# Kernel tuning notes

Hardware: AMD Instinct MI355X
Metric: run time of the kernel (lower is better)

## Reference

```python
import jax, jax.numpy as jnp
import numpy as np

D = 1024      # d_model
H = 16        # nhead
DH = 64       # qkv_dim (per-head)
FF = 4096     # dim_feedforward
EPS = 1e-5


def layer_norm(x, g, b):
    mu = jnp.mean(x, axis=-1, keepdims=True)
    var = jnp.mean(jnp.square(x - mu), axis=-1, keepdims=True)
    return (x - mu) * jax.lax.rsqrt(var + EPS) * g + b


def setup_inputs() -> dict:
    key = jax.random.key(0)
    ks = jax.random.split(key, 17)
    s = 0.02
    inp = {
        "src": jax.random.normal(ks[0], (2, 2048, D), jnp.float32),
        "qw": jax.random.normal(ks[1], (H * DH, D), jnp.float32) * s,
        "qb": jnp.zeros((H * DH,), jnp.float32),
        "kw": jax.random.normal(ks[2], (H * DH, D), jnp.float32) * s,
        "kb": jnp.zeros((H * DH,), jnp.float32),
        "vw": jax.random.normal(ks[3], (H * DH, D), jnp.float32) * s,
        "vb": jnp.zeros((H * DH,), jnp.float32),
        "ow": jax.random.normal(ks[4], (D, H * DH), jnp.float32) * s,
        "ob": jnp.zeros((D,), jnp.float32),
        "w1": jax.random.normal(ks[5], (FF, D), jnp.float32) * s,
        "b1": jnp.zeros((FF,), jnp.float32),
        "w2": jax.random.normal(ks[6], (D, FF), jnp.float32) * s,
        "b2": jnp.zeros((D,), jnp.float32),
        "g1": jnp.ones((D,), jnp.float32),
        "beta1": jnp.zeros((D,), jnp.float32),
        "g2": jnp.ones((D,), jnp.float32),
        "beta2": jnp.zeros((D,), jnp.float32),
    }
    return inp


def _attn(x, qw, qb, kw, kb, vw, vb, ow, ob):
    B, S, _ = x.shape
    scale = 1.0 / np.sqrt(DH)
    # projections -> [B, H, S, DH]
    q = (x @ qw.T + qb).reshape(B, S, H, DH).transpose(0, 2, 1, 3)
    k = (x @ kw.T + kb).reshape(B, S, H, DH).transpose(0, 2, 1, 3)
    v = (x @ vw.T + vb).reshape(B, S, H, DH).transpose(0, 2, 1, 3)
    scores = jnp.einsum('bhsd,bhtd->bhst', q, k) * scale
    attn = jax.nn.softmax(scores, axis=-1)
    out = jnp.einsum('bhst,bhtd->bhsd', attn, v)  # [B,H,S,DH]
    out = out.transpose(0, 2, 1, 3).reshape(B, S, H * DH)
    return out @ ow.T + ob


def reference(src, qw, qb, kw, kb, vw, vb, ow, ob, w1, b1, w2, b2, g1, beta1, g2, beta2):
    x = src
    # post-LN (norm_first=False), dropout=0 (eval)
    x = layer_norm(x + _attn(x, qw, qb, kw, kb, vw, vb, ow, ob), g1, beta1)
    ff = jax.nn.relu(x @ w1.T + b1) @ w2.T + b2
    x = layer_norm(x + ff, g2, beta2)
    return x
```

## Files before the change

### kernel.cpp

```cpp
#include <hip/hip_runtime.h>

typedef unsigned short bf16_t;
typedef unsigned short u16x8 __attribute__((ext_vector_type(8)));
typedef unsigned short u16x4 __attribute__((ext_vector_type(4)));
typedef float f32x4 __attribute__((ext_vector_type(4)));

#define D_MODEL 1024
#define NHEAD 16
#define DHEAD 64
#define FF_DIM 4096
#define SEQ 2048
#define BATCH 2
#define LOG2E 1.44269504088896340736f
#define EXP2F(x) __builtin_amdgcn_exp2f(x)

#define GLOAD_LDS16(gp, lp)                                          \
  __builtin_amdgcn_global_load_lds(                                  \
      (const __attribute__((address_space(1))) void*)(gp),           \
      (__attribute__((address_space(3))) void*)(lp), 16, 0, 0)

static __device__ __forceinline__ float bf2f(bf16_t b) {
  union { unsigned u; float f; } x;
  x.u = ((unsigned)b) << 16;
  return x.f;
}
static __device__ __forceinline__ bf16_t f2bf(float f) {
  union { float f; unsigned u; } x;
  x.f = f;
  unsigned r = (x.u + 0x7fffu + ((x.u >> 16) & 1u)) >> 16;
  return (bf16_t)r;
}
static __device__ __forceinline__ int cvtpk(float lo, float hi) {
  int r;
  asm("v_cvt_pk_bf16_f32 %0, %1, %2" : "=v"(r) : "v"(lo), "v"(hi));
  return r;
}
static __device__ __forceinline__ f32x4 mfma16(u16x8 a, u16x8 b, f32x4 c) {
  return __builtin_amdgcn_mfma_f32_16x16x32_bf16(a, b, c, 0, 0, 0);
}
static __device__ __forceinline__ u16x8 load8_f32(const float* q) {
  const float4 v0 = *(const float4*)(q);
  const float4 v1 = *(const float4*)(q + 4);
  u16x8 r;
  r[0] = f2bf(v0.x); r[1] = f2bf(v0.y); r[2] = f2bf(v0.z); r[3] = f2bf(v0.w);
  r[4] = f2bf(v1.x); r[5] = f2bf(v1.y); r[6] = f2bf(v1.z); r[7] = f2bf(v1.w);
  return r;
}

__global__ __launch_bounds__(256) void cvt_f32_bf16(
    const float* __restrict__ in, bf16_t* __restrict__ out, long n) {
  const long i = ((long)blockIdx.x * 256 + threadIdx.x) * 8;
  if (i < n) *(u16x8*)(out + i) = load8_f32(in + i);
}

template <int SMODE>
__global__ __launch_bounds__(256) void gemm_lds(
    const bf16_t* __restrict__ A, const bf16_t* __restrict__ W,
    const float* __restrict__ bq_, const float* __restrict__ bk_,
    const float* __restrict__ bv_, bf16_t* __restrict__ C0,
    bf16_t* __restrict__ C1, bf16_t* __restrict__ C2,
    bf16_t* __restrict__ C3,
    int N, int Kseg, long lda, long ldw, int relu, float qscale,
    int gxs) {
  __shared__ bf16_t As[128 * 32];
  __shared__ bf16_t Bs[128 * 32];
  const int tid = threadIdx.x;
  const int lane = tid & 63;
  const int w = tid >> 6;
  const int wr = w >> 1, wc = w & 1;
  const int g = lane >> 4, c = lane & 15;

  const int per = (int)gridDim.x >> 3;
  const int gt = (blockIdx.x & 7) * per + (blockIdx.x >> 3);
  const int u = gt & 31;
  const int st = gt >> 5;
  const int sx = st % gxs;
  const int t2 = st / gxs;
  const int sy = t2 & 7;
  const int z = t2 >> 3;
  const long bm = (long)(sy * 4 + (u & 3)) * 128;
  const long bn = (long)(sx * 8 + (u >> 2)) * 128;
  const long koff = (long)z * Kseg;

  f32x4 acc[4][4];
#pragma unroll
  for (int i = 0; i < 4; ++i)
#pragma unroll
    for (int j = 0; j < 4; ++j) acc[i][j] = (f32x4){0.f, 0.f, 0.f, 0.f};

  for (int k0 = 0; k0 < Kseg; k0 += 32) {
    __syncthreads();
#pragma unroll
    for (int ld = 0; ld < 2; ++ld) {
      const int ch = ld * 256 + tid;
      GLOAD_LDS16(A + (bm + (ch >> 2)) * lda + koff + k0 + (ch & 3) * 8,
                  As + (ld * 256 + w * 64) * 8);
    }
#pragma unroll
    for (int ld = 0; ld < 2; ++ld) {
      const int ch = ld * 256 + tid;
      GLOAD_LDS16(W + (bn + (ch >> 2)) * ldw + koff + k0 + (ch & 3) * 8,
                  Bs + (ld * 256 + w * 64) * 8);
    }
    __syncthreads();
    u16x8 af[4], bfv[4];
#pragma unroll
    for (int i = 0; i < 4; ++i)
      af[i] = *(const u16x8*)(As + (wr * 64 + i * 16 + c) * 32 + g * 8);
#pragma unroll
    for (int j = 0; j < 4; ++j)
      bfv[j] = *(const u16x8*)(Bs + (wc * 64 + j * 16 + c) * 32 + g * 8);
    __builtin_amdgcn_s_setprio(1);
#pragma unroll
    for (int i = 0; i < 4; ++i)
#pragma unroll
      for (int j = 0; j < 4; ++j) acc[i][j] = mfma16(af[i], bfv[j], acc[i][j]);
    __builtin_amdgcn_s_setprio(0);
  }

  bf16_t* __restrict__ pp =
      (z == 0) ? C0 : (z == 1) ? C1 : (z == 2) ? C2 : C3;
#pragma unroll
  for (int i = 0; i < 4; ++i) {
#pragma unroll
    for (int j = 0; j < 4; ++j) {
      const int nn = (int)bn + wc * 64 + j * 16 + c;
#pragma unroll
      for (int r = 0; r < 4; ++r) {
        const int mm = (int)bm + wr * 64 + i * 16 + g * 4 + r;
        if (SMODE == 0) {
          float v = acc[i][j][r] + bq_[nn];
          if (relu) v = fmaxf(v, 0.f);
          C0[(long)mm * N + nn] = f2bf(v);
        } else if (SMODE == 4) {
          pp[(long)mm * N + nn] = f2bf(acc[i][j][r]);
        } else {
          const int seg = nn >> 10;
          const int col = nn & 1023;
          const int h = col >> 6, dh = col & 63;
          const int b = mm >> 11, s = mm & 2047;
          if (seg == 0) {
            const float v = (acc[i][j][r] + bq_[col]) * qscale;
            C0[((((long)b * NHEAD + h) * SEQ + s) << 6) + dh] = f2bf(v);
          } else if (seg == 1) {
            const float v = acc[i][j][r] + bk_[col];
            C1[((((long)b * NHEAD + h) * SEQ + s) << 6) + dh] = f2bf(v);
          } else {
            const float v = acc[i][j][r] + bv_[col];
            C2[(((long)b * NHEAD + h) * DHEAD + dh) * SEQ + s] = f2bf(v);
          }
        }
      }
    }
  }
}

template <int KEY>
static __device__ __forceinline__ void stage_tile(
    const bf16_t* __restrict__ gbase, long rstride, bf16_t* lds,
    int tid, int w) {
#pragma unroll
  for (int i = 0; i < 2; ++i) {
    const int row = i * 32 + (tid >> 3);
    const int key = KEY ? ((row & 3) | ((row & 8) >> 1)) : (row & 7);
    const int c4 = (tid & 7) ^ key;
    GLOAD_LDS16(gbase + (long)row * rstride + c4 * 8,
                lds + (i * 256 + w * 64) * 8);
  }
}

__global__ __launch_bounds__(256, 2) void attn_fwd(
    const bf16_t* __restrict__ Q, const bf16_t* __restrict__ K,
    const bf16_t* __restrict__ Vt, bf16_t* __restrict__ O) {
  __shared__ bf16_t Ks0[64 * 64];
  __shared__ bf16_t Ks1[64 * 64];
  __shared__ bf16_t Vs0[64 * 64];
  __shared__ bf16_t Vs1[64 * 64];
  const int tid = threadIdx.x;
  const int lane = tid & 63;
  const int w = tid >> 6;
  const int g = lane >> 4, c = lane & 15;
  const int lb = blockIdx.x;
  const int xcd = lb & 7, sl = lb >> 3;
  const int bh = xcd * 4 + (sl >> 4);
  const int q0 = (sl & 15) * 128 + w * 32;
  const bf16_t* Qb = Q + (long)bh * SEQ * DHEAD;
  const bf16_t* Kb = K + (long)bh * SEQ * DHEAD;
  const bf16_t* Vb = Vt + (long)bh * DHEAD * SEQ;

  u16x8 bq[2][2];
#pragma unroll
  for (int qh = 0; qh < 2; ++qh) {
    bq[qh][0] = *(const u16x8*)(Qb + (q0 + qh * 16 + c) * DHEAD + g * 8);
    bq[qh][1] = *(const u16x8*)(Qb + (q0 + qh * 16 + c) * DHEAD + 32 + g * 8);
  }

  float m0 = -1e30f, m1 = -1e30f, lp0 = 0.f, lp1 = 0.f;
  f32x4 oacc[4][2];
#pragma unroll
  for (int d = 0; d < 4; ++d)
#pragma unroll
    for (int qh = 0; qh < 2; ++qh) oacc[d][qh] = (f32x4){0.f, 0.f, 0.f, 0.f};

  const int ck = c & 7;
  const int pr = ((c >> 2) << 3) | (c & 3);

  for (int t0 = 0; t0 < SEQ; t0 += 128) {
    __syncthreads();
    stage_tile<1>(Kb + (long)t0 * DHEAD, DHEAD, Ks0, tid, w);
    stage_tile<1>(Kb + (long)(t0 + 64) * DHEAD, DHEAD, Ks1, tid, w);
    stage_tile<0>(Vb + t0, SEQ, Vs0, tid, w);
    stage_tile<0>(Vb + t0 + 64, SEQ, Vs1, tid, w);
    __syncthreads();

#pragma unroll
    for (int sub = 0; sub < 2; ++sub) {
      const bf16_t* Ks = sub ? Ks1 : Ks0;
      const bf16_t* Vs = sub ? Vs1 : Vs0;

      f32x4 s[2][2][2];
#pragma unroll
      for (int tt = 0; tt < 2; ++tt) {
        const int rowA = (tt * 32 + pr) * 64;
        const int rowC = (tt * 32 + pr + 4) * 64;
        const u16x8 kA = *(const u16x8*)(Ks + rowA + (g ^ ck) * 8);
        const u16x8 kB = *(const u16x8*)(Ks + rowA + ((4 + g) ^ ck) * 8);
        const u16x8 kC = *(const u16x8*)(Ks + rowC + (g ^ ck) * 8);
        const u16x8 kD = *(const u16x8*)(Ks + rowC + ((4 + g) ^ ck) * 8);
        __builtin_amdgcn_s_setprio(1);
#pragma unroll
        for (int qh = 0; qh < 2; ++qh) {
          s[tt][0][qh] = mfma16(kA, bq[qh][0], (f32x4){0.f, 0.f, 0.f, 0.f});
          s[tt][0][qh] = mfma16(kB, bq[qh][1], s[tt][0][qh]);
          s[tt][1][qh] = mfma16(kC, bq[qh][0], (f32x4){0.f, 0.f, 0.f, 0.f});
          s[tt][1][qh] = mfma16(kD, bq[qh][1], s[tt][1][qh]);
        }
        __builtin_amdgcn_s_setprio(0);
      }

      float pmv[2];
#pragma unroll
      for (int qh = 0; qh < 2; ++qh) {
        float pm = s[0][0][qh][0];
#pragma unroll
        for (int tt = 0; tt < 2; ++tt)
#pragma unroll
          for (int pi = 0; pi < 2; ++pi)
#pragma unroll
            for (int r = 0; r < 4; ++r) pm = fmaxf(pm, s[tt][pi][qh][r]);
        pm = fmaxf(pm, __shfl_xor(pm, 16));
        pm = fmaxf(pm, __shfl_xor(pm, 32));
        pmv[qh] = pm;
      }
      if (!__all(pmv[0] <= m0 + 8.f && pmv[1] <= m1 + 8.f)) {
        const float mn0 = fmaxf(m0, pmv[0]);
        const float mn1 = fmaxf(m1, pmv[1]);
        const float f0 = EXP2F(m0 - mn0);
        const float f1 = EXP2F(m1 - mn1);
        m0 = mn0; m1 = mn1;
        lp0 *= f0; lp1 *= f1;
        float fb0[4], fb1[4];
#pragma unroll
        for (int r = 0; r < 4; ++r) {
          fb0[r] = __shfl(f0, 4 * g + r);
          fb1[r] = __shfl(f1, 4 * g + r);
        }
#pragma unroll
        for (int d = 0; d < 4; ++d)
#pragma unroll
          for (int r = 0; r < 4; ++r) {
            oacc[d][0][r] *= fb0[r];
            oacc[d][1][r] *= fb1[r];
          }
      }
      float ts0 = 0.f, ts1 = 0.f;
#pragma unroll
      for (int tt = 0; tt < 2; ++tt)
#pragma unroll
        for (int pi = 0; pi < 2; ++pi)
#pragma unroll
          for (int r = 0; r < 4; ++r) {
            s[tt][pi][0][r] = EXP2F(s[tt][pi][0][r] - m0);
            s[tt][pi][1][r] = EXP2F(s[tt][pi][1][r] - m1);
            ts0 += s[tt][pi][0][r];
            ts1 += s[tt][pi][1][r];
          }
      lp0 += ts0;
      lp1 += ts1;

      union { int u[4]; u16x8 v; } pu[2][2];
#pragma unroll
      for (int qh = 0; qh < 2; ++qh)
#pragma unroll
        for (int tt = 0; tt < 2; ++tt) {
          pu[qh][tt].u[0] = cvtpk(s[tt][0][qh][0], s[tt][0][qh][1]);
          pu[qh][tt].u[1] = cvtpk(s[tt][0][qh][2], s[tt][0][qh][3]);
          pu[qh][tt].u[2] = cvtpk(s[tt][1][qh][0], s[tt][1][qh][1]);
          pu[qh][tt].u[3] = cvtpk(s[tt][1][qh][2], s[tt][1][qh][3]);
        }

#pragma unroll
      for (int d = 0; d < 4; ++d) {
        const int rowb = (d * 16 + c) * 64;
        const u16x8 v0 = *(const u16x8*)(Vs + rowb + ((g ^ ck)) * 8);
        const u16x8 v1 = *(const u16x8*)(Vs + rowb + (((4 + g) ^ ck)) * 8);
        __builtin_amdgcn_s_setprio(1);
        oacc[d][0] = mfma16(pu[0][0].v, v0, oacc[d][0]);
        oacc[d][0] = mfma16(pu[0][1].v, v1, oacc[d][0]);
        oacc[d][1] = mfma16(pu[1][0].v, v0, oacc[d][1]);
        oacc[d][1] = mfma16(pu[1][1].v, v1, oacc[d][1]);
        __builtin_amdgcn_s_setprio(0);
      }
    }
  }

  const int b = bh >> 4, h = bh & 15;
#pragma unroll
  for (int qh = 0; qh < 2; ++qh) {
    float lt = qh ? lp1 : lp0;
    lt += __shfl_xor(lt, 16);
    lt += __shfl_xor(lt, 32);
#pragma unroll
    for (int r = 0; r < 4; ++r) {
      const float inv = 1.f / __shfl(lt, 4 * g + r);
      const long base =
          ((long)b * SEQ + q0 + qh * 16 + g * 4 + r) * D_MODEL + h * DHEAD;
#pragma unroll
      for (int d = 0; d < 4; ++d)
        O[base + d * 16 + c] = f2bf(oacc[d][qh][r] * inv);
    }
  }
}

template <int XF32, int OUTF32, int YPART>
__global__ __launch_bounds__(256) void add_ln(
    const void* __restrict__ X, const bf16_t* __restrict__ Y0,
    const bf16_t* __restrict__ Y1, const bf16_t* __restrict__ Y2,
    const bf16_t* __restrict__ Y3, const float* __restrict__ ybias,
    const float* __restrict__ gamma, const float* __restrict__ beta,
    void* __restrict__ Out) {
  __shared__ float red[2][4];
  const int tid = threadIdx.x;
  const int lane = tid & 63, w = tid >> 6;
  const long base = (long)blockIdx.x * D_MODEL;

  float xv[4];
  if (XF32) {
    const float4 t = *(const float4*)((const float*)X + base + tid * 4);
    xv[0] = t.x; xv[1] = t.y; xv[2] = t.z; xv[3] = t.w;
  } else {
    const u16x4 t = *(const u16x4*)((const bf16_t*)X + base + tid * 4);
#pragma unroll
    for (int i = 0; i < 4; ++i) xv[i] = bf2f(t[i]);
  }
  float yv[4];
  if (YPART) {
    const u16x4 t0 = *(const u16x4*)(Y0 + base + tid * 4);
    const u16x4 t1 = *(const u16x4*)(Y1 + base + tid * 4);
    const u16x4 t2 = *(const u16x4*)(Y2 + base + tid * 4);
    const u16x4 t3 = *(const u16x4*)(Y3 + base + tid * 4);
    const float4 bb = *(const float4*)(ybias + tid * 4);
#pragma unroll
    for (int i = 0; i < 4; ++i)
      yv[i] = ((bf2f(t0[i]) + bf2f(t1[i])) + (bf2f(t2[i]) + bf2f(t3[i]))) +
              ((const float*)&bb)[i];
  } else {
    const u16x4 t = *(const u16x4*)(Y0 + base + tid * 4);
#pragma unroll
    for (int i = 0; i < 4; ++i) yv[i] = bf2f(t[i]);
  }
  float v[4], s = 0.f, s2 = 0.f;
#pragma unroll
  for (int i = 0; i < 4; ++i) {
    const float t = xv[i] + yv[i];
    v[i] = t;
    s += t;
    s2 += t * t;
  }
#pragma unroll
  for (int off = 32; off; off >>= 1) {
    s += __shfl_xor(s, off);
    s2 += __shfl_xor(s2, off);
  }
  if (lane == 0) { red[0][w] = s; red[1][w] = s2; }
  __syncthreads();
  s = red[0][0] + red[0][1] + red[0][2] + red[0][3];
  s2 = red[1][0] + red[1][1] + red[1][2] + red[1][3];
  const float mu = s * (1.f / D_MODEL);
  const float var = s2 * (1.f / D_MODEL) - mu * mu;
  const float inv = rsqrtf(var + 1e-5f);
  const float4 gv = *(const float4*)(gamma + tid * 4);
  const float4 bv = *(const float4*)(beta + tid * 4);
  const float o0 = (v[0] - mu) * inv * gv.x + bv.x;
  const float o1 = (v[1] - mu) * inv * gv.y + bv.y;
  const float o2 = (v[2] - mu) * inv * gv.z + bv.z;
  const float o3 = (v[3] - mu) * inv * gv.w + bv.w;
  if (OUTF32) {
    float4 ov; ov.x = o0; ov.y = o1; ov.z = o2; ov.w = o3;
    *(float4*)((float*)Out + base + tid * 4) = ov;
  } else {
    u16x4 ov;
    ov[0] = f2bf(o0); ov[1] = f2bf(o1); ov[2] = f2bf(o2); ov[3] = f2bf(o3);
    *(u16x4*)((bf16_t*)Out + base + tid * 4) = ov;
  }
}

extern "C" void kernel_launch(void* const* d_in, const int* in_sizes, int n_in,
                              void* d_out, int out_size, void* d_ws, size_t ws_size,
                              hipStream_t stream) {
  const float* src = (const float*)d_in[0];
  const float* qw = (const float*)d_in[1];
  const float* qb = (const float*)d_in[2];
  const float* kw = (const float*)d_in[3];
  const float* kb = (const float*)d_in[4];
  const float* vw = (const float*)d_in[5];
  const float* vb = (const float*)d_in[6];
  const float* ow = (const float*)d_in[7];
  const float* ob = (const float*)d_in[8];
  const float* w1 = (const float*)d_in[9];
  const float* b1 = (const float*)d_in[10];
  const float* w2 = (const float*)d_in[11];
  const float* b2 = (const float*)d_in[12];
  const float* gam1 = (const float*)d_in[13];
  const float* bet1 = (const float*)d_in[14];
  const float* gam2 = (const float*)d_in[15];
  const float* bet2 = (const float*)d_in[16];

  char* ws = (char*)d_ws;
  const long MB = 1024 * 1024;
  bf16_t* Qw   = (bf16_t*)(ws + 0 * MB);
  bf16_t* Kw   = (bf16_t*)(ws + 8 * MB);
  bf16_t* Vt   = (bf16_t*)(ws + 16 * MB);
  bf16_t* A1   = (bf16_t*)(ws + 24 * MB);
  bf16_t* X1   = (bf16_t*)(ws + 40 * MB);
  bf16_t* srcB = (bf16_t*)(ws + 48 * MB);
  bf16_t* Wqkv = (bf16_t*)(ws + 56 * MB);
  bf16_t* OWb  = (bf16_t*)(ws + 62 * MB);
  bf16_t* W1b  = (bf16_t*)(ws + 64 * MB);
  bf16_t* W2b  = (bf16_t*)(ws + 72 * MB);
  bf16_t* Poa  = (bf16_t*)(ws + 0 * MB);
  bf16_t* Pob  = (bf16_t*)(ws + 8 * MB);
  bf16_t* Poc  = (bf16_t*)(ws + 16 * MB);
  bf16_t* Pod  = (bf16_t*)(ws + 48 * MB);
  bf16_t* F1   = (bf16_t*)(ws + 0 * MB);
  bf16_t* Pfa  = (bf16_t*)(ws + 48 * MB);
  bf16_t* Pfb  = (bf16_t*)(ws + 56 * MB);
  bf16_t* Pfc  = (bf16_t*)(ws + 64 * MB);
  bf16_t* Pfd  = (bf16_t*)(ws + 80 * MB);

  const int M = BATCH * SEQ;
  dim3 blk(256);
  const float qscale = 0.125f * LOG2E;
  const long n1M = 1024 * 1024;

  cvt_f32_bf16<<<dim3(2048), blk, 0, stream>>>(src, srcB, (long)M * D_MODEL);
  cvt_f32_bf16<<<dim3(512), blk, 0, stream>>>(qw, Wqkv, n1M);
  cvt_f32_bf16<<<dim3(512), blk, 0, stream>>>(kw, Wqkv + n1M, n1M);
  cvt_f32_bf16<<<dim3(512), blk, 0, stream>>>(vw, Wqkv + 2 * n1M, n1M);
  cvt_f32_bf16<<<dim3(512), blk, 0, stream>>>(ow, OWb, n1M);
  cvt_f32_bf16<<<dim3(2048), blk, 0, stream>>>(w1, W1b, 4 * n1M);
  cvt_f32_bf16<<<dim3(2048), blk, 0, stream>>>(w2, W2b, 4 * n1M);

  gemm_lds<3><<<dim3(768), blk, 0, stream>>>(
      srcB, Wqkv, qb, kb, vb, Qw, Kw, Vt, (bf16_t*)0,
      3072, 1024, 1024, 1024, 0, qscale, 3);
  attn_fwd<<<dim3(512), blk, 0, stream>>>(Qw, Kw, Vt, A1);
  gemm_lds<4><<<dim3(1024), blk, 0, stream>>>(
      A1, OWb, ob, ob, ob, Poa, Pob, Poc, Pod,
      1024, 256, 1024, 1024, 0, 1.f, 1);
  add_ln<1, 0, 1><<<dim3(M), blk, 0, stream>>>(
      src, Poa, Pob, Poc, Pod, ob, gam1, bet1, X1);
  gemm_lds<0><<<dim3(1024), blk, 0, stream>>>(
      X1, W1b, b1, b1, b1, F1, F1, F1, (bf16_t*)0,
      4096, 1024, 1024, 1024, 1, 1.f, 4);
  gemm_lds<4><<<dim3(1024), blk, 0, stream>>>(
      F1, W2b, b2, b2, b2, Pfa, Pfb, Pfc, Pfd,
      1024, 1024, 4096, 4096, 0, 1.f, 1);
  add_ln<0, 1, 1><<<dim3(M), blk, 0, stream>>>(
      X1, Pfa, Pfb, Pfc, Pfd, b2, gam2, bet2, d_out);
}
```

Baseline: 272.5 us.

## Merge f32-to-bf16 conversions into one launch and double GEMM K-tile with XOR-swizzled LDS

Replaces seven separate fp32-to-bf16 conversion launches with a single kernel that picks its source and destination by block index, removing launch overhead and tail gaps. The GEMM K-tile grows from 32 to 64, which halves the number of sync/load iterations and doubles LDS usage per block. A row-based XOR swizzle is applied to the 16-byte chunks, both when writing to LDS and when reading from it, to avoid bank conflicts. The larger LDS footprint may lower occupancy.

```diff
diff --git a/kernel.cpp b/kernel.cpp
--- a/kernel.cpp
+++ b/kernel.cpp
@@ -47,10 +47,31 @@
   return r;
 }
 
-__global__ __launch_bounds__(256) void cvt_f32_bf16(
-    const float* __restrict__ in, bf16_t* __restrict__ out, long n) {
-  const long i = ((long)blockIdx.x * 256 + threadIdx.x) * 8;
-  if (i < n) *(u16x8*)(out + i) = load8_f32(in + i);
+__global__ __launch_bounds__(256) void cvt_all(
+    const float* __restrict__ src, bf16_t* __restrict__ dsrc,
+    const float* __restrict__ qw, const float* __restrict__ kw,
+    const float* __restrict__ vw, const float* __restrict__ ow,
+    bf16_t* __restrict__ wqkv, bf16_t* __restrict__ owb,
+    const float* __restrict__ w1, bf16_t* __restrict__ w1b,
+    const float* __restrict__ w2, bf16_t* __restrict__ w2b) {
+  const int b = blockIdx.x;
+  const float* s;
+  bf16_t* d;
+  long off;
+  if (b < 2048) {
+    s = src; d = dsrc; off = (long)b * 2048;
+  } else if (b < 4096) {
+    const int seg = (b - 2048) >> 9, r = (b - 2048) & 511;
+    s = seg == 0 ? qw : seg == 1 ? kw : seg == 2 ? vw : ow;
+    d = (seg == 3) ? owb : wqkv + (long)seg * 1048576;
+    off = (long)r * 2048;
+  } else if (b < 6144) {
+    s = w1; d = w1b; off = (long)(b - 4096) * 2048;
+  } else {
+    s = w2; d = w2b; off = (long)(b - 6144) * 2048;
+  }
+  const long i = off + threadIdx.x * 8;
+  *(u16x8*)(d + i) = load8_f32(s + i);
 }
 
 template <int SMODE>
@@ -62,8 +83,8 @@
     bf16_t* __restrict__ C3,
     int N, int Kseg, long lda, long ldw, int relu, float qscale,
     int gxs) {
-  __shared__ bf16_t As[128 * 32];
-  __shared__ bf16_t Bs[128 * 32];
+  __shared__ bf16_t As[128 * 64];
+  __shared__ bf16_t Bs[128 * 64];
   const int tid = threadIdx.x;
   const int lane = tid & 63;
   const int w = tid >> 6;
@@ -88,34 +109,46 @@
 #pragma unroll
     for (int j = 0; j < 4; ++j) acc[i][j] = (f32x4){0.f, 0.f, 0.f, 0.f};
 
-  for (int k0 = 0; k0 < Kseg; k0 += 32) {
+  const int ckey = c & 7;
+
+  for (int k0 = 0; k0 < Kseg; k0 += 64) {
     __syncthreads();
 #pragma unroll
-    for (int ld = 0; ld < 2; ++ld) {
+    for (int ld = 0; ld < 4; ++ld) {
       const int ch = ld * 256 + tid;
-      GLOAD_LDS16(A + (bm + (ch >> 2)) * lda + koff + k0 + (ch & 3) * 8,
+      const int row = ch >> 3;
+      const int cc = (ch & 7) ^ (row & 7);
+      GLOAD_LDS16(A + (bm + row) * lda + koff + k0 + cc * 8,
                   As + (ld * 256 + w * 64) * 8);
     }
 #pragma unroll
-    for (int ld = 0; ld < 2; ++ld) {
+    for (int ld = 0; ld < 4; ++ld) {
       const int ch = ld * 256 + tid;
-      GLOAD_LDS16(W + (bn + (ch >> 2)) * ldw + koff + k0 + (ch & 3) * 8,
+      const int row = ch >> 3;
+      const int cc = (ch & 7) ^ (row & 7);
+      GLOAD_LDS16(W + (bn + row) * ldw + koff + k0 + cc * 8,
                   Bs + (ld * 256 + w * 64) * 8);
     }
     __syncthreads();
-    u16x8 af[4], bfv[4];
-#pragma unroll
-    for (int i = 0; i < 4; ++i)
-      af[i] = *(const u16x8*)(As + (wr * 64 + i * 16 + c) * 32 + g * 8);
-#pragma unroll
-    for (int j = 0; j < 4; ++j)
-      bfv[j] = *(const u16x8*)(Bs + (wc * 64 + j * 16 + c) * 32 + g * 8);
-    __builtin_amdgcn_s_setprio(1);
-#pragma unroll
-    for (int i = 0; i < 4; ++i)
-#pragma unroll
-      for (int j = 0; j < 4; ++j) acc[i][j] = mfma16(af[i], bfv[j], acc[i][j]);
-    __builtin_amdgcn_s_setprio(0);
+#pragma unroll
+    for (int kk = 0; kk < 2; ++kk) {
+      u16x8 af[4], bfv[4];
+#pragma unroll
+      for (int i = 0; i < 4; ++i)
+        af[i] = *(const u16x8*)(
+            As + ((wr * 64 + i * 16 + c) * 8 + ((kk * 4 + g) ^ ckey)) * 8);
+#pragma unroll
+      for (int j = 0; j < 4; ++j)
+        bfv[j] = *(const u16x8*)(
+            Bs + ((wc * 64 + j * 16 + c) * 8 + ((kk * 4 + g) ^ ckey)) * 8);
+      __builtin_amdgcn_s_setprio(1);
+#pragma unroll
+      for (int i = 0; i < 4; ++i)
+#pragma unroll
+        for (int j = 0; j < 4; ++j)
+          acc[i][j] = mfma16(af[i], bfv[j], acc[i][j]);
+      __builtin_amdgcn_s_setprio(0);
+    }
   }
 
   bf16_t* __restrict__ pp =
@@ -451,15 +484,9 @@
   const int M = BATCH * SEQ;
   dim3 blk(256);
   const float qscale = 0.125f * LOG2E;
-  const long n1M = 1024 * 1024;
-
-  cvt_f32_bf16<<<dim3(2048), blk, 0, stream>>>(src, srcB, (long)M * D_MODEL);
-  cvt_f32_bf16<<<dim3(512), blk, 0, stream>>>(qw, Wqkv, n1M);
-  cvt_f32_bf16<<<dim3(512), blk, 0, stream>>>(kw, Wqkv + n1M, n1M);
-  cvt_f32_bf16<<<dim3(512), blk, 0, stream>>>(vw, Wqkv + 2 * n1M, n1M);
-  cvt_f32_bf16<<<dim3(512), blk, 0, stream>>>(ow, OWb, n1M);
-  cvt_f32_bf16<<<dim3(2048), blk, 0, stream>>>(w1, W1b, 4 * n1M);
-  cvt_f32_bf16<<<dim3(2048), blk, 0, stream>>>(w2, W2b, 4 * n1M);
+
+  cvt_all<<<dim3(8192), blk, 0, stream>>>(
+      src, srcB, qw, kw, vw, ow, Wqkv, OWb, w1, W1b, w2, W2b);
 
   gemm_lds<3><<<dim3(768), blk, 0, stream>>>(
       srcB, Wqkv, qb, kb, vb, Qw, Kw, Vt, (bf16_t*)0,
```

Result: faster. 247.1 us, median of 2 (-9.3%).
